# Kernel optimization log

Hardware: AMD Instinct MI355X
Metric: run time of the kernel (lower is better)

## Reference

```python
import jax, jax.numpy as jnp
import numpy as np

B, H, W, D, C = 2, 20, 20, 20, 64
R = 8  # reduction_ratio


def setup_inputs() -> dict:
    key = jax.random.key(0)
    k1, k2, k3, k4, k5 = jax.random.split(key, 5)
    x = jax.random.normal(k1, (B, H, W, D, C), dtype=jnp.float32)
    Wf = jax.random.normal(k2, (C, C // R), dtype=jnp.float32) * 0.1
    Wg = jax.random.normal(k3, (C, C // R), dtype=jnp.float32) * 0.1
    Wh = jax.random.normal(k4, (C, C), dtype=jnp.float32) * 0.1
    gamma = jax.random.normal(k5, (1,), dtype=jnp.float32)
    return {"x": x, "Wf": Wf, "Wg": Wg, "Wh": Wh, "gamma": gamma}


def reference(x, Wf, Wg, Wh, gamma):
    b, h, w, d, c = x.shape
    n = h * w * d
    x_flat = x.reshape(b, n, c)                       # [B, N, C]
    # 1x1x1 Conv3D with no bias == per-voxel linear projection
    f = x_flat @ Wf                                   # [B, N, C/R]
    g = x_flat @ Wg                                   # [B, N, C/R]
    hh = x_flat @ Wh                                  # [B, N, C]
    # s[b, i, j] = <g_i, f_j>
    s = jnp.einsum('bie,bje->bij', g, f)              # [B, N, N]
    beta = jax.nn.softmax(s, axis=-1)
    o = jnp.einsum('bij,bjc->bic', beta, hh)          # [B, N, C]
    o = o.reshape(b, h, w, d, c)
    return gamma * o + x
```

## Files before the change

### kernel.cpp

```cpp
#include <hip/hip_runtime.h>
#include <stdint.h>
#include <stddef.h>

#define NB 2
#define NN 8000
#define NC 64
#define NKT 500
#define STAGE_KT 5
#define LOG2E 1.44269504f
#define NQB 63

#define KV_BYTES  ((size_t)NB * NKT * 2560)
#define GB_OFF    KV_BYTES
#define GB_BYTES  ((size_t)NB * NKT * 64 * 8)
#define PML_OFF   (GB_OFF + GB_BYTES)

__host__ __device__ constexpr size_t pml_bytes(int s) { return (size_t)NB * NKT * s * 16 * 4; }
__host__ __device__ constexpr size_t po_off(int s)    { return PML_OFF + pml_bytes(s); }
__host__ __device__ constexpr size_t po_bytes(int s)  { return (size_t)NB * NKT * s * 2048; }

typedef float f32x4 __attribute__((ext_vector_type(4)));
typedef short s16x4 __attribute__((ext_vector_type(4)));

__device__ inline short f2bf(float f) {
    union { float f; uint32_t u; } v; v.f = f;
    uint32_t u = v.u + 0x7FFFu + ((v.u >> 16) & 1u);
    return (short)(u >> 16);
}
__device__ inline float fexp2(float x) { return __builtin_amdgcn_exp2f(x); }
__device__ inline uint32_t pack_trunc(uint32_t a_lo, uint32_t b_hi) {
    return __builtin_amdgcn_perm(b_hi, a_lo, 0x07060302u);
}

__global__ __launch_bounds__(256) void proj_kernel(
    const float* __restrict__ x,
    const float* __restrict__ Wf,
    const float* __restrict__ Wg,
    const float* __restrict__ Wh,
    uint8_t* __restrict__ ws)
{
    __shared__ float Wh_s[64][68];
    __shared__ float Wf_s[64][8];
    __shared__ float Wg_s[64][8];
    __shared__ float x_s[4][16][68];
    __shared__ float h_s[4][16][68];

    const int tid = threadIdx.x;
    const int L = tid & 63, w = tid >> 6;
    const int lane16 = L & 15, g4 = L >> 4;

    for (int i = tid; i < 64 * 64; i += 256) Wh_s[i >> 6][i & 63] = Wh[i];
    for (int i = tid; i < 64 * 8; i += 256) {
        Wf_s[i >> 3][i & 7] = Wf[i] * LOG2E;
        Wg_s[i >> 3][i & 7] = Wg[i];
    }

    const int ktg = blockIdx.x * 4 + w;
    const int b = ktg / NKT, ktb = ktg % NKT;
    const float* xsrc = x + ((size_t)b * NN + (size_t)ktb * 16) * NC;

    #pragma unroll
    for (int i = 0; i < 4; i++) {
        int F = i * 256 + L * 4;
        f32x4 v = *(const f32x4*)(xsrc + F);
        *(f32x4*)&x_s[w][F >> 6][F & 63] = v;
    }
    __syncthreads();

    uint2* kv2 = (uint2*)ws;
    uint4* kv4 = (uint4*)ws;
    uint2* gB  = (uint2*)(ws + GB_OFF);
    const size_t kt = (size_t)(b * NKT + ktb);

    {
        float fa0 = 0, fa1 = 0, fa2 = 0, fa3 = 0;
        float ga0 = 0, ga1 = 0, ga2 = 0, ga3 = 0;
        const int d0 = (g4 & 1) * 4;
        #pragma unroll 4
        for (int k = 0; k < 64; k++) {
            float xv = x_s[w][lane16][k];
            fa0 += xv * Wf_s[k][d0 + 0]; fa1 += xv * Wf_s[k][d0 + 1];
            fa2 += xv * Wf_s[k][d0 + 2]; fa3 += xv * Wf_s[k][d0 + 3];
            ga0 += xv * Wg_s[k][d0 + 0]; ga1 += xv * Wg_s[k][d0 + 1];
            ga2 += xv * Wg_s[k][d0 + 2]; ga3 += xv * Wg_s[k][d0 + 3];
        }
        const bool valid = (g4 < 2);
        union { s16x4 v; uint2 u; } fp, gp;
        fp.v[0] = valid ? f2bf(fa0) : (short)0;
        fp.v[1] = valid ? f2bf(fa1) : (short)0;
        fp.v[2] = valid ? f2bf(fa2) : (short)0;
        fp.v[3] = valid ? f2bf(fa3) : (short)0;
        gp.v[0] = valid ? f2bf(ga0) : (short)0;
        gp.v[1] = valid ? f2bf(ga1) : (short)0;
        gp.v[2] = valid ? f2bf(ga2) : (short)0;
        gp.v[3] = valid ? f2bf(ga3) : (short)0;
        kv2[kt * 320 + L] = fp.u;
        gB[kt * 64 + L] = gp.u;
    }

    {
        float ha[16];
        #pragma unroll
        for (int i = 0; i < 16; i++) ha[i] = 0.f;
        const int c0 = g4 * 16;
        for (int k = 0; k < 64; k++) {
            float xv = x_s[w][lane16][k];
            const f32x4 w0 = *(const f32x4*)&Wh_s[k][c0 + 0];
            const f32x4 w1 = *(const f32x4*)&Wh_s[k][c0 + 4];
            const f32x4 w2 = *(const f32x4*)&Wh_s[k][c0 + 8];
            const f32x4 w3 = *(const f32x4*)&Wh_s[k][c0 + 12];
            #pragma unroll
            for (int e = 0; e < 4; e++) {
                ha[e]      += xv * w0[e];
                ha[4 + e]  += xv * w1[e];
                ha[8 + e]  += xv * w2[e];
                ha[12 + e] += xv * w3[e];
            }
        }
        #pragma unroll
        for (int i = 0; i < 4; i++) {
            f32x4 t; t[0] = ha[4*i]; t[1] = ha[4*i+1]; t[2] = ha[4*i+2]; t[3] = ha[4*i+3];
            *(f32x4*)&h_s[w][lane16][c0 + 4 * i] = t;
        }
    }
    __syncthreads();

    {
        union { s16x4 v; uint2 u; } hp[4];
        #pragma unroll
        for (int cb = 0; cb < 4; cb++)
            #pragma unroll
            for (int e = 0; e < 4; e++)
                hp[cb].v[e] = f2bf(h_s[w][g4 * 4 + e][cb * 16 + lane16]);
        uint4 h01, h23;
        h01.x = hp[0].u.x; h01.y = hp[0].u.y; h01.z = hp[1].u.x; h01.w = hp[1].u.y;
        h23.x = hp[2].u.x; h23.y = hp[2].u.y; h23.z = hp[3].u.x; h23.w = hp[3].u.y;
        kv4[kt * 160 + 32 + L] = h01;
        kv4[kt * 160 + 96 + L] = h23;
    }
}

template<int SPLITT>
__global__ __launch_bounds__(256, 4) void attn_kernel(
    const uint8_t* __restrict__ ws_in,
    uint8_t* __restrict__ ws_out)
{
    constexpr int TPS = NKT / SPLITT;
    constexpr int NST = TPS / STAGE_KT;
    __shared__ uint4 kvs4[STAGE_KT * 160];
    const uint2* kvs2 = (const uint2*)kvs4;

    const int tid = threadIdx.x;
    const int L = tid & 63, w = tid >> 6;
    const int lane16 = L & 15, g4 = L >> 4;

    const int bid = blockIdx.x;
    const int qblk = bid % NQB;
    const int bs = bid / NQB;
    const int b = bs / SPLITT, s = bs % SPLITT;
    const int qta = qblk * 8 + w * 2;
    const int qtb = qta + 1;
    const bool va = (qta < NKT), vb = (qtb < NKT);
    const int qla = va ? qta : 0, qlb = vb ? qtb : 0;

    const uint4* kv4 = (const uint4*)ws_in;
    const uint2* gB  = (const uint2*)(ws_in + GB_OFF);
    float* part_l = (float*)(ws_out + PML_OFF);
    uint2* part_O = (uint2*)(ws_out + po_off(SPLITT));

    s16x4 bga, bgb;
    { union { uint2 u; s16x4 v; } t; t.u = gB[(size_t)(b * NKT + qla) * 64 + L]; bga = t.v; }
    { union { uint2 u; s16x4 v; } t; t.u = gB[(size_t)(b * NKT + qlb) * 64 + L]; bgb = t.v; }

    float l_a = 0.f, l_b = 0.f;
    const f32x4 zz = {0, 0, 0, 0};
    f32x4 oa0 = {0,0,0,0}, oa1 = {0,0,0,0}, oa2 = {0,0,0,0}, oa3 = {0,0,0,0};
    f32x4 ob0 = {0,0,0,0}, ob1 = {0,0,0,0}, ob2 = {0,0,0,0}, ob3 = {0,0,0,0};

    const int kt0 = s * TPS;
    const uint4* stage_base = kv4 + (size_t)(b * NKT + kt0) * 160;

    for (int st = 0; st < NST; st++) {
        __syncthreads();
        {
            const uint4* src = stage_base + (size_t)st * (STAGE_KT * 160);
            uint4 tmp[3];
            #pragma unroll
            for (int i = 0; i < 3; i++) tmp[i] = src[tid + i * 256];
            uint4 tailv;
            if (tid < 32) tailv = src[768 + tid];
            #pragma unroll
            for (int i = 0; i < 3; i++) kvs4[tid + i * 256] = tmp[i];
            if (tid < 32) kvs4[768 + tid] = tailv;
        }
        __syncthreads();

        #pragma unroll
        for (int ktl = 0; ktl < STAGE_KT; ktl++) {
            s16x4 af;
            { union { uint2 u; s16x4 v; } t; t.u = kvs2[ktl * 320 + L]; af = t.v; }

            f32x4 sva = __builtin_amdgcn_mfma_f32_16x16x16bf16_1k(af, bga, zz, 0, 0, 0);
            f32x4 svb = __builtin_amdgcn_mfma_f32_16x16x16bf16_1k(af, bgb, zz, 0, 0, 0);

            float pa0 = fexp2(sva[0]), pa1 = fexp2(sva[1]);
            float pa2 = fexp2(sva[2]), pa3 = fexp2(sva[3]);
            l_a += (pa0 + pa1) + (pa2 + pa3);
            float pb0 = fexp2(svb[0]), pb1 = fexp2(svb[1]);
            float pb2 = fexp2(svb[2]), pb3 = fexp2(svb[3]);
            l_b += (pb0 + pb1) + (pb2 + pb3);

            union { float f; uint32_t u; } c0, c1, c2, c3;
            union { uint2 u; s16x4 v; } ppa, ppb;
            c0.f = pa0; c1.f = pa1; c2.f = pa2; c3.f = pa3;
            ppa.u.x = pack_trunc(c0.u, c1.u);
            ppa.u.y = pack_trunc(c2.u, c3.u);
            c0.f = pb0; c1.f = pb1; c2.f = pb2; c3.f = pb3;
            ppb.u.x = pack_trunc(c0.u, c1.u);
            ppb.u.y = pack_trunc(c2.u, c3.u);

            union { uint4 q; uint2 d[2]; } hu01, hu23;
            hu01.q = kvs4[ktl * 160 + 32 + L];
            hu23.q = kvs4[ktl * 160 + 96 + L];
            s16x4 h0, h1, h2, h3;
            { union { uint2 u; s16x4 v; } t; t.u = hu01.d[0]; h0 = t.v; }
            { union { uint2 u; s16x4 v; } t; t.u = hu01.d[1]; h1 = t.v; }
            { union { uint2 u; s16x4 v; } t; t.u = hu23.d[0]; h2 = t.v; }
            { union { uint2 u; s16x4 v; } t; t.u = hu23.d[1]; h3 = t.v; }

            oa0 = __builtin_amdgcn_mfma_f32_16x16x16bf16_1k(ppa.v, h0, oa0, 0, 0, 0);
            oa1 = __builtin_amdgcn_mfma_f32_16x16x16bf16_1k(ppa.v, h1, oa1, 0, 0, 0);
            oa2 = __builtin_amdgcn_mfma_f32_16x16x16bf16_1k(ppa.v, h2, oa2, 0, 0, 0);
            oa3 = __builtin_amdgcn_mfma_f32_16x16x16bf16_1k(ppa.v, h3, oa3, 0, 0, 0);
            ob0 = __builtin_amdgcn_mfma_f32_16x16x16bf16_1k(ppb.v, h0, ob0, 0, 0, 0);
            ob1 = __builtin_amdgcn_mfma_f32_16x16x16bf16_1k(ppb.v, h1, ob1, 0, 0, 0);
            ob2 = __builtin_amdgcn_mfma_f32_16x16x16bf16_1k(ppb.v, h2, ob2, 0, 0, 0);
            ob3 = __builtin_amdgcn_mfma_f32_16x16x16bf16_1k(ppb.v, h3, ob3, 0, 0, 0);
        }
    }

    if (va) {
        float lsum = l_a;
        lsum += __shfl_xor(lsum, 16);
        lsum += __shfl_xor(lsum, 32);
        const size_t pslot = (size_t)(b * NKT + qta) * SPLITT + s;
        if (g4 == 0) part_l[pslot * 16 + lane16] = lsum;
        uint2* obase = part_O + pslot * 256;
        #pragma unroll
        for (int r = 0; r < 4; r++) {
            const int row = g4 * 4 + r;
            union { s16x4 v; uint2 u; } ou;
            ou.v[0] = f2bf(oa0[r]); ou.v[1] = f2bf(oa1[r]);
            ou.v[2] = f2bf(oa2[r]); ou.v[3] = f2bf(oa3[r]);
            obase[row * 16 + lane16] = ou.u;
        }
    }
    if (vb) {
        float lsum = l_b;
        lsum += __shfl_xor(lsum, 16);
        lsum += __shfl_xor(lsum, 32);
        const size_t pslot = (size_t)(b * NKT + qtb) * SPLITT + s;
        if (g4 == 0) part_l[pslot * 16 + lane16] = lsum;
        uint2* obase = part_O + pslot * 256;
        #pragma unroll
        for (int r = 0; r < 4; r++) {
            const int row = g4 * 4 + r;
            union { s16x4 v; uint2 u; } ou;
            ou.v[0] = f2bf(ob0[r]); ou.v[1] = f2bf(ob1[r]);
            ou.v[2] = f2bf(ob2[r]); ou.v[3] = f2bf(ob3[r]);
            obase[row * 16 + lane16] = ou.u;
        }
    }
}

template<int SPLITT>
__global__ __launch_bounds__(256) void combine_kernel(
    const float* __restrict__ x,
    const float* __restrict__ gammap,
    const uint8_t* __restrict__ ws,
    float* __restrict__ out)
{
    const int idx = blockIdx.x * 256 + threadIdx.x;
    const int j = idx & 15;
    const int row_g = idx >> 4;
    const int b = row_g / NN;
    const int row = row_g - b * NN;
    const int qt = row >> 4, q = row & 15;

    const float* part_l = (const float*)(ws + PML_OFF);
    const uint2* part_O = (const uint2*)(ws + po_off(SPLITT));
    const size_t pbase = (size_t)(b * NKT + qt) * SPLITT;

    float Lsum = 0.f, O0 = 0.f, O1 = 0.f, O2 = 0.f, O3 = 0.f;
    #pragma unroll
    for (int s = 0; s < SPLITT; s++) {
        Lsum += part_l[(pbase + s) * 16 + q];
        uint2 u = part_O[(pbase + s) * 256 + q * 16 + j];
        O0 += __uint_as_float(u.x << 16);
        O1 += __uint_as_float(u.x & 0xffff0000u);
        O2 += __uint_as_float(u.y << 16);
        O3 += __uint_as_float(u.y & 0xffff0000u);
    }
    const float inv = gammap[0] / Lsum;
    const size_t base = (size_t)row_g * 64 + j;
    out[base +  0] = O0 * inv + x[base +  0];
    out[base + 16] = O1 * inv + x[base + 16];
    out[base + 32] = O2 * inv + x[base + 32];
    out[base + 48] = O3 * inv + x[base + 48];
}

extern "C" void kernel_launch(void* const* d_in, const int* in_sizes, int n_in,
                              void* d_out, int out_size, void* d_ws, size_t ws_size,
                              hipStream_t stream) {
    const float* x     = (const float*)d_in[0];
    const float* Wf    = (const float*)d_in[1];
    const float* Wg    = (const float*)d_in[2];
    const float* Wh    = (const float*)d_in[3];
    const float* gamma = (const float*)d_in[4];
    float* out = (float*)d_out;
    uint8_t* ws = (uint8_t*)d_ws;

    proj_kernel<<<250, 256, 0, stream>>>(x, Wf, Wg, Wh, ws);

    const size_t need20 = po_off(20) + po_bytes(20);
    const size_t need10 = po_off(10) + po_bytes(10);
    if (ws_size >= need20) {
        attn_kernel<20><<<NB * NQB * 20, 256, 0, stream>>>(ws, ws);
        combine_kernel<20><<<(NB * NN * 16) / 256, 256, 0, stream>>>(x, gamma, ws, out);
    } else if (ws_size >= need10) {
        attn_kernel<10><<<NB * NQB * 10, 256, 0, stream>>>(ws, ws);
        combine_kernel<10><<<(NB * NN * 16) / 256, 256, 0, stream>>>(x, gamma, ws, out);
    } else {
        attn_kernel<5><<<NB * NQB * 5, 256, 0, stream>>>(ws, ws);
        combine_kernel<5><<<(NB * NN * 16) / 256, 256, 0, stream>>>(x, gamma, ws, out);
    }
}
```

Before: 56.54 us.

## Split projection waves by role and add 25-way key split for attention

The projection kernel now handles two key tiles per block instead of four. Within each tile, one wave computes the f/g projections and another computes the h projection, so the grid doubles to 500 blocks and each wave does less serial work. The attention launcher also gains a 25-way key-split variant when the workspace is large enough, which adds more blocks but more partial results for the combine step to read and merge.

```diff
diff --git a/kernel.cpp b/kernel.cpp
--- a/kernel.cpp
+++ b/kernel.cpp
@@ -42,12 +42,14 @@
     __shared__ float Wh_s[64][68];
     __shared__ float Wf_s[64][8];
     __shared__ float Wg_s[64][8];
-    __shared__ float x_s[4][16][68];
-    __shared__ float h_s[4][16][68];
+    __shared__ float x_s[2][16][68];
+    __shared__ float h_s[2][16][68];
 
     const int tid = threadIdx.x;
     const int L = tid & 63, w = tid >> 6;
     const int lane16 = L & 15, g4 = L >> 4;
+    const int ktl = w >> 1;
+    const int role = w & 1;
 
     for (int i = tid; i < 64 * 64; i += 256) Wh_s[i >> 6][i & 63] = Wh[i];
     for (int i = tid; i < 64 * 8; i += 256) {
@@ -55,30 +57,29 @@
         Wg_s[i >> 3][i & 7] = Wg[i];
     }
 
-    const int ktg = blockIdx.x * 4 + w;
-    const int b = ktg / NKT, ktb = ktg % NKT;
-    const float* xsrc = x + ((size_t)b * NN + (size_t)ktb * 16) * NC;
-
     #pragma unroll
-    for (int i = 0; i < 4; i++) {
-        int F = i * 256 + L * 4;
-        f32x4 v = *(const f32x4*)(xsrc + F);
-        *(f32x4*)&x_s[w][F >> 6][F & 63] = v;
+    for (int kk = 0; kk < 2; kk++) {
+        const int kg = blockIdx.x * 2 + kk;
+        const int bb = kg / NKT, kb = kg % NKT;
+        const float* xsrc = x + ((size_t)bb * NN + (size_t)kb * 16) * NC;
+        const int F = tid * 4;
+        *(f32x4*)&x_s[kk][F >> 6][F & 63] = *(const f32x4*)(xsrc + F);
     }
     __syncthreads();
 
+    const int ktg = blockIdx.x * 2 + ktl;
     uint2* kv2 = (uint2*)ws;
     uint4* kv4 = (uint4*)ws;
     uint2* gB  = (uint2*)(ws + GB_OFF);
-    const size_t kt = (size_t)(b * NKT + ktb);
-
-    {
+    const size_t kt = (size_t)ktg;
+
+    if (role == 0) {
         float fa0 = 0, fa1 = 0, fa2 = 0, fa3 = 0;
         float ga0 = 0, ga1 = 0, ga2 = 0, ga3 = 0;
         const int d0 = (g4 & 1) * 4;
         #pragma unroll 4
         for (int k = 0; k < 64; k++) {
-            float xv = x_s[w][lane16][k];
+            float xv = x_s[ktl][lane16][k];
             fa0 += xv * Wf_s[k][d0 + 0]; fa1 += xv * Wf_s[k][d0 + 1];
             fa2 += xv * Wf_s[k][d0 + 2]; fa3 += xv * Wf_s[k][d0 + 3];
             ga0 += xv * Wg_s[k][d0 + 0]; ga1 += xv * Wg_s[k][d0 + 1];
@@ -96,15 +97,13 @@
         gp.v[3] = valid ? f2bf(ga3) : (short)0;
         kv2[kt * 320 + L] = fp.u;
         gB[kt * 64 + L] = gp.u;
-    }
-
-    {
+    } else {
         float ha[16];
         #pragma unroll
         for (int i = 0; i < 16; i++) ha[i] = 0.f;
         const int c0 = g4 * 16;
         for (int k = 0; k < 64; k++) {
-            float xv = x_s[w][lane16][k];
+            float xv = x_s[ktl][lane16][k];
             const f32x4 w0 = *(const f32x4*)&Wh_s[k][c0 + 0];
             const f32x4 w1 = *(const f32x4*)&Wh_s[k][c0 + 4];
             const f32x4 w2 = *(const f32x4*)&Wh_s[k][c0 + 8];
@@ -120,18 +119,18 @@
         #pragma unroll
         for (int i = 0; i < 4; i++) {
             f32x4 t; t[0] = ha[4*i]; t[1] = ha[4*i+1]; t[2] = ha[4*i+2]; t[3] = ha[4*i+3];
-            *(f32x4*)&h_s[w][lane16][c0 + 4 * i] = t;
+            *(f32x4*)&h_s[ktl][lane16][c0 + 4 * i] = t;
         }
     }
     __syncthreads();
 
-    {
+    if (role == 1) {
         union { s16x4 v; uint2 u; } hp[4];
         #pragma unroll
         for (int cb = 0; cb < 4; cb++)
             #pragma unroll
             for (int e = 0; e < 4; e++)
-                hp[cb].v[e] = f2bf(h_s[w][g4 * 4 + e][cb * 16 + lane16]);
+                hp[cb].v[e] = f2bf(h_s[ktl][g4 * 4 + e][cb * 16 + lane16]);
         uint4 h01, h23;
         h01.x = hp[0].u.x; h01.y = hp[0].u.y; h01.z = hp[1].u.x; h01.w = hp[1].u.y;
         h23.x = hp[2].u.x; h23.y = hp[2].u.y; h23.z = hp[3].u.x; h23.w = hp[3].u.y;
@@ -320,11 +319,15 @@
     float* out = (float*)d_out;
     uint8_t* ws = (uint8_t*)d_ws;
 
-    proj_kernel<<<250, 256, 0, stream>>>(x, Wf, Wg, Wh, ws);
-
+    proj_kernel<<<500, 256, 0, stream>>>(x, Wf, Wg, Wh, ws);
+
+    const size_t need25 = po_off(25) + po_bytes(25);
     const size_t need20 = po_off(20) + po_bytes(20);
     const size_t need10 = po_off(10) + po_bytes(10);
-    if (ws_size >= need20) {
+    if (ws_size >= need25) {
+        attn_kernel<25><<<NB * NQB * 25, 256, 0, stream>>>(ws, ws);
+        combine_kernel<25><<<(NB * NN * 16) / 256, 256, 0, stream>>>(x, gamma, ws, out);
+    } else if (ws_size >= need20) {
         attn_kernel<20><<<NB * NQB * 20, 256, 0, stream>>>(ws, ws);
         combine_kernel<20><<<(NB * NN * 16) / 256, 256, 0, stream>>>(x, gamma, ws, out);
     } else if (ws_size >= need10) {
```

Result: slower. 59.10 us (+4.5%).

## Process four query tiles per wave to double K/V reuse from shared memory

Applied to the files above, without the earlier changes.

Each wave now handles four 16-row query tiles instead of two, so each block covers 16 query tiles and the grid's query-block count drops from 63 to 32. Every K/V fragment loaded from LDS feeds twice as many MFMAs, cutting LDS traffic and staging loads per unit of work. In exchange the wave holds about twice as many accumulator registers, which may hurt occupancy under the 4-blocks-per-CU launch bound, and the grid has half as many blocks. The inner loop's unroll pragma was also removed.

```diff
diff --git a/kernel.cpp b/kernel.cpp
--- a/kernel.cpp
+++ b/kernel.cpp
@@ -8,7 +8,7 @@
 #define NKT 500
 #define STAGE_KT 5
 #define LOG2E 1.44269504f
-#define NQB 63
+#define NQB 32
 
 #define KV_BYTES  ((size_t)NB * NKT * 2560)
 #define GB_OFF    KV_BYTES
@@ -140,6 +140,16 @@
     }
 }
 
+#define SM_PACK(sv, l, pp) do { \
+    float p0 = fexp2(sv[0]), p1 = fexp2(sv[1]); \
+    float p2 = fexp2(sv[2]), p3 = fexp2(sv[3]); \
+    l += (p0 + p1) + (p2 + p3); \
+    union { float f; uint32_t u; } q0, q1, q2, q3; \
+    q0.f = p0; q1.f = p1; q2.f = p2; q3.f = p3; \
+    pp.u.x = pack_trunc(q0.u, q1.u); \
+    pp.u.y = pack_trunc(q2.u, q3.u); \
+} while (0)
+
 template<int SPLITT>
 __global__ __launch_bounds__(256, 4) void attn_kernel(
     const uint8_t* __restrict__ ws_in,
@@ -158,24 +168,27 @@
     const int qblk = bid % NQB;
     const int bs = bid / NQB;
     const int b = bs / SPLITT, s = bs % SPLITT;
-    const int qta = qblk * 8 + w * 2;
-    const int qtb = qta + 1;
-    const bool va = (qta < NKT), vb = (qtb < NKT);
-    const int qla = va ? qta : 0, qlb = vb ? qtb : 0;
+    const int qt0 = qblk * 16 + w * 4;
 
     const uint4* kv4 = (const uint4*)ws_in;
     const uint2* gB  = (const uint2*)(ws_in + GB_OFF);
     float* part_l = (float*)(ws_out + PML_OFF);
     uint2* part_O = (uint2*)(ws_out + po_off(SPLITT));
 
-    s16x4 bga, bgb;
-    { union { uint2 u; s16x4 v; } t; t.u = gB[(size_t)(b * NKT + qla) * 64 + L]; bga = t.v; }
-    { union { uint2 u; s16x4 v; } t; t.u = gB[(size_t)(b * NKT + qlb) * 64 + L]; bgb = t.v; }
-
-    float l_a = 0.f, l_b = 0.f;
+    const bool vA = (qt0 + 0 < NKT), vB = (qt0 + 1 < NKT);
+    const bool vC = (qt0 + 2 < NKT), vD = (qt0 + 3 < NKT);
+    s16x4 bgA, bgB, bgC, bgD;
+    { union { uint2 u; s16x4 v; } t; t.u = gB[(size_t)(b * NKT + (vA ? qt0 + 0 : 0)) * 64 + L]; bgA = t.v; }
+    { union { uint2 u; s16x4 v; } t; t.u = gB[(size_t)(b * NKT + (vB ? qt0 + 1 : 0)) * 64 + L]; bgB = t.v; }
+    { union { uint2 u; s16x4 v; } t; t.u = gB[(size_t)(b * NKT + (vC ? qt0 + 2 : 0)) * 64 + L]; bgC = t.v; }
+    { union { uint2 u; s16x4 v; } t; t.u = gB[(size_t)(b * NKT + (vD ? qt0 + 3 : 0)) * 64 + L]; bgD = t.v; }
+
+    float l_A = 0.f, l_B = 0.f, l_C = 0.f, l_D = 0.f;
     const f32x4 zz = {0, 0, 0, 0};
-    f32x4 oa0 = {0,0,0,0}, oa1 = {0,0,0,0}, oa2 = {0,0,0,0}, oa3 = {0,0,0,0};
-    f32x4 ob0 = {0,0,0,0}, ob1 = {0,0,0,0}, ob2 = {0,0,0,0}, ob3 = {0,0,0,0};
+    f32x4 oA0 = {0,0,0,0}, oA1 = {0,0,0,0}, oA2 = {0,0,0,0}, oA3 = {0,0,0,0};
+    f32x4 oB0 = {0,0,0,0}, oB1 = {0,0,0,0}, oB2 = {0,0,0,0}, oB3 = {0,0,0,0};
+    f32x4 oC0 = {0,0,0,0}, oC1 = {0,0,0,0}, oC2 = {0,0,0,0}, oC3 = {0,0,0,0};
+    f32x4 oD0 = {0,0,0,0}, oD1 = {0,0,0,0}, oD2 = {0,0,0,0}, oD3 = {0,0,0,0};
 
     const int kt0 = s * TPS;
     const uint4* stage_base = kv4 + (size_t)(b * NKT + kt0) * 160;
@@ -195,29 +208,20 @@
         }
         __syncthreads();
 
-        #pragma unroll
         for (int ktl = 0; ktl < STAGE_KT; ktl++) {
             s16x4 af;
             { union { uint2 u; s16x4 v; } t; t.u = kvs2[ktl * 320 + L]; af = t.v; }
 
-            f32x4 sva = __builtin_amdgcn_mfma_f32_16x16x16bf16_1k(af, bga, zz, 0, 0, 0);
-            f32x4 svb = __builtin_amdgcn_mfma_f32_16x16x16bf16_1k(af, bgb, zz, 0, 0, 0);
-
-            float pa0 = fexp2(sva[0]), pa1 = fexp2(sva[1]);
-            float pa2 = fexp2(sva[2]), pa3 = fexp2(sva[3]);
-            l_a += (pa0 + pa1) + (pa2 + pa3);
-            float pb0 = fexp2(svb[0]), pb1 = fexp2(svb[1]);
-            float pb2 = fexp2(svb[2]), pb3 = fexp2(svb[3]);
-            l_b += (pb0 + pb1) + (pb2 + pb3);
-
-            union { float f; uint32_t u; } c0, c1, c2, c3;
-            union { uint2 u; s16x4 v; } ppa, ppb;
-            c0.f = pa0; c1.f = pa1; c2.f = pa2; c3.f = pa3;
-            ppa.u.x = pack_trunc(c0.u, c1.u);
-            ppa.u.y = pack_trunc(c2.u, c3.u);
-            c0.f = pb0; c1.f = pb1; c2.f = pb2; c3.f = pb3;
-            ppb.u.x = pack_trunc(c0.u, c1.u);
-            ppb.u.y = pack_trunc(c2.u, c3.u);
+            f32x4 svA = __builtin_amdgcn_mfma_f32_16x16x16bf16_1k(af, bgA, zz, 0, 0, 0);
+            f32x4 svB = __builtin_amdgcn_mfma_f32_16x16x16bf16_1k(af, bgB, zz, 0, 0, 0);
+            f32x4 svC = __builtin_amdgcn_mfma_f32_16x16x16bf16_1k(af, bgC, zz, 0, 0, 0);
+            f32x4 svD = __builtin_amdgcn_mfma_f32_16x16x16bf16_1k(af, bgD, zz, 0, 0, 0);
+
+            union { uint2 u; s16x4 v; } ppA, ppB, ppC, ppD;
+            SM_PACK(svA, l_A, ppA);
+            SM_PACK(svB, l_B, ppB);
+            SM_PACK(svC, l_C, ppC);
+            SM_PACK(svD, l_D, ppD);
 
             union { uint4 q; uint2 d[2]; } hu01, hu23;
             hu01.q = kvs4[ktl * 160 + 32 + L];
@@ -228,49 +232,49 @@
             { union { uint2 u; s16x4 v; } t; t.u = hu23.d[0]; h2 = t.v; }
             { union { uint2 u; s16x4 v; } t; t.u = hu23.d[1]; h3 = t.v; }
 
-            oa0 = __builtin_amdgcn_mfma_f32_16x16x16bf16_1k(ppa.v, h0, oa0, 0, 0, 0);
-            oa1 = __builtin_amdgcn_mfma_f32_16x16x16bf16_1k(ppa.v, h1, oa1, 0, 0, 0);
-            oa2 = __builtin_amdgcn_mfma_f32_16x16x16bf16_1k(ppa.v, h2, oa2, 0, 0, 0);
-            oa3 = __builtin_amdgcn_mfma_f32_16x16x16bf16_1k(ppa.v, h3, oa3, 0, 0, 0);
-            ob0 = __builtin_amdgcn_mfma_f32_16x16x16bf16_1k(ppb.v, h0, ob0, 0, 0, 0);
-            ob1 = __builtin_amdgcn_mfma_f32_16x16x16bf16_1k(ppb.v, h1, ob1, 0, 0, 0);
-            ob2 = __builtin_amdgcn_mfma_f32_16x16x16bf16_1k(ppb.v, h2, ob2, 0, 0, 0);
-            ob3 = __builtin_amdgcn_mfma_f32_16x16x16bf16_1k(ppb.v, h3, ob3, 0, 0, 0);
-        }
-    }
-
-    if (va) {
-        float lsum = l_a;
-        lsum += __shfl_xor(lsum, 16);
-        lsum += __shfl_xor(lsum, 32);
-        const size_t pslot = (size_t)(b * NKT + qta) * SPLITT + s;
-        if (g4 == 0) part_l[pslot * 16 + lane16] = lsum;
-        uint2* obase = part_O + pslot * 256;
-        #pragma unroll
-        for (int r = 0; r < 4; r++) {
-            const int row = g4 * 4 + r;
-            union { s16x4 v; uint2 u; } ou;
-            ou.v[0] = f2bf(oa0[r]); ou.v[1] = f2bf(oa1[r]);
-            ou.v[2] = f2bf(oa2[r]); ou.v[3] = f2bf(oa3[r]);
-            obase[row * 16 + lane16] = ou.u;
-        }
-    }
-    if (vb) {
-        float lsum = l_b;
-        lsum += __shfl_xor(lsum, 16);
-        lsum += __shfl_xor(lsum, 32);
-        const size_t pslot = (size_t)(b * NKT + qtb) * SPLITT + s;
-        if (g4 == 0) part_l[pslot * 16 + lane16] = lsum;
-        uint2* obase = part_O + pslot * 256;
-        #pragma unroll
-        for (int r = 0; r < 4; r++) {
-            const int row = g4 * 4 + r;
-            union { s16x4 v; uint2 u; } ou;
-            ou.v[0] = f2bf(ob0[r]); ou.v[1] = f2bf(ob1[r]);
-            ou.v[2] = f2bf(ob2[r]); ou.v[3] = f2bf(ob3[r]);
-            obase[row * 16 + lane16] = ou.u;
-        }
-    }
+            oA0 = __builtin_amdgcn_mfma_f32_16x16x16bf16_1k(ppA.v, h0, oA0, 0, 0, 0);
+            oA1 = __builtin_amdgcn_mfma_f32_16x16x16bf16_1k(ppA.v, h1, oA1, 0, 0, 0);
+            oA2 = __builtin_amdgcn_mfma_f32_16x16x16bf16_1k(ppA.v, h2, oA2, 0, 0, 0);
+            oA3 = __builtin_amdgcn_mfma_f32_16x16x16bf16_1k(ppA.v, h3, oA3, 0, 0, 0);
+            oB0 = __builtin_amdgcn_mfma_f32_16x16x16bf16_1k(ppB.v, h0, oB0, 0, 0, 0);
+            oB1 = __builtin_amdgcn_mfma_f32_16x16x16bf16_1k(ppB.v, h1, oB1, 0, 0, 0);
+            oB2 = __builtin_amdgcn_mfma_f32_16x16x16bf16_1k(ppB.v, h2, oB2, 0, 0, 0);
+            oB3 = __builtin_amdgcn_mfma_f32_16x16x16bf16_1k(ppB.v, h3, oB3, 0, 0, 0);
+            oC0 = __builtin_amdgcn_mfma_f32_16x16x16bf16_1k(ppC.v, h0, oC0, 0, 0, 0);
+            oC1 = __builtin_amdgcn_mfma_f32_16x16x16bf16_1k(ppC.v, h1, oC1, 0, 0, 0);
+            oC2 = __builtin_amdgcn_mfma_f32_16x16x16bf16_1k(ppC.v, h2, oC2, 0, 0, 0);
+            oC3 = __builtin_amdgcn_mfma_f32_16x16x16bf16_1k(ppC.v, h3, oC3, 0, 0, 0);
+            oD0 = __builtin_amdgcn_mfma_f32_16x16x16bf16_1k(ppD.v, h0, oD0, 0, 0, 0);
+            oD1 = __builtin_amdgcn_mfma_f32_16x16x16bf16_1k(ppD.v, h1, oD1, 0, 0, 0);
+            oD2 = __builtin_amdgcn_mfma_f32_16x16x16bf16_1k(ppD.v, h2, oD2, 0, 0, 0);
+            oD3 = __builtin_amdgcn_mfma_f32_16x16x16bf16_1k(ppD.v, h3, oD3, 0, 0, 0);
+        }
+    }
+
+#define STORE_QT(QTOFF, VALID, LV, O0, O1, O2, O3) do { \
+    float ls = LV; \
+    ls += __shfl_xor(ls, 16); \
+    ls += __shfl_xor(ls, 32); \
+    if (VALID) { \
+        const size_t pslot = (size_t)(b * NKT + qt0 + (QTOFF)) * SPLITT + s; \
+        if (g4 == 0) part_l[pslot * 16 + lane16] = ls; \
+        uint2* obase = part_O + pslot * 256; \
+        _Pragma("unroll") \
+        for (int r = 0; r < 4; r++) { \
+            const int row = g4 * 4 + r; \
+            union { s16x4 v; uint2 u; } ou; \
+            ou.v[0] = f2bf(O0[r]); ou.v[1] = f2bf(O1[r]); \
+            ou.v[2] = f2bf(O2[r]); ou.v[3] = f2bf(O3[r]); \
+            obase[row * 16 + lane16] = ou.u; \
+        } \
+    } \
+} while (0)
+
+    STORE_QT(0, vA, l_A, oA0, oA1, oA2, oA3);
+    STORE_QT(1, vB, l_B, oB0, oB1, oB2, oB3);
+    STORE_QT(2, vC, l_C, oC0, oC1, oC2, oC3);
+    STORE_QT(3, vD, l_D, oD0, oD1, oD2, oD3);
+#undef STORE_QT
 }
 
 template<int SPLITT>
```

Result: slower. 183.8 us (+225.1%).
